# Performance work log

Hardware: AMD Instinct MI355X
Metric: run time of the kernel (lower is better)

Reference implementation:

```python
import jax, jax.numpy as jnp
import numpy as np
from jax import lax

NUM_VARS = 16384
NUM_CHECKS = 8192
BATCH = 32
MAX_ITER = 15
H_DENSITY = 0.001  # ~8 ones per column, LDPC-like Tanner graph


def setup_inputs() -> dict:
    key = jax.random.key(0)
    k_h, k_s, k_l = jax.random.split(key, 3)
    # Sparse binary parity-check matrix represented densely (same math).
    parity_matrix = (jax.random.uniform(k_h, (NUM_CHECKS, NUM_VARS)) < H_DENSITY).astype(jnp.float32)
    syndrome = jax.random.randint(k_s, (BATCH, NUM_CHECKS), 0, 2).astype(jnp.float32)
    channel_llrs = jax.random.normal(k_l, (BATCH, NUM_VARS), dtype=jnp.float32)
    w_vc = jnp.ones((1,), dtype=jnp.float32)
    w_cv = jnp.ones((1,), dtype=jnp.float32)
    damping = jnp.float32(0.5)
    return {
        "syndrome": syndrome,
        "parity_matrix": parity_matrix,
        "channel_llrs": channel_llrs,
        "w_vc": w_vc,
        "w_cv": w_cv,
        "damping": damping,
    }


def reference(syndrome, parity_matrix, channel_llrs, w_vc, w_cv, damping):
    # syndrome: (B, C); parity_matrix H: (C, V); channel_llrs: (B, V)
    s_sign = 1.0 - 2.0 * syndrome  # (B, C)

    def body(v_beliefs, _):
        # v -> c: sparse.mm(H, v^T)^T == v @ H^T  -> (B, C)
        v_to_c = w_vc * (v_beliefs @ parity_matrix.T)
        c_msg = s_sign * jnp.tanh(v_to_c * 0.5)  # (B, C)
        # c -> v: sparse.mm(H^T, c^T)^T == c @ H  -> (B, V)
        c_to_v = w_cv * (c_msg @ parity_matrix)
        v_new = damping * v_beliefs + (1.0 - damping) * (channel_llrs + c_to_v)
        return v_new, None

    v_beliefs, _ = lax.scan(body, channel_llrs, None, length=MAX_ITER)
    return jax.nn.sigmoid(-v_beliefs)  # (B, V) bit-flip probabilities
```

## Files before the change

### kernel.cpp

```cpp
#include <hip/hip_runtime.h>


#define C_NUM 8192
#define V_NUM 16384
#define B_NUM 32
#define ROW_SLOTS 40
#define COL_SLOTS 24

#define NBLK 256
#define NTHR 1024
#define NTH (NBLK * NTHR)

typedef unsigned short u16;
typedef unsigned int u32;
typedef unsigned long long u64;

#define ZERO_WORDS ((C_NUM * 4 + V_NUM * 4 + C_NUM * ROW_SLOTS * 2 + V_NUM * COL_SLOTS * 2) / 4)
#define NBAR 31

__device__ __forceinline__ float agent_ldf(const float* p) {
    return __hip_atomic_load(p, __ATOMIC_RELAXED, __HIP_MEMORY_SCOPE_AGENT);
}
__device__ __forceinline__ void agent_stf(float* p, float v) {
    __hip_atomic_store(p, v, __ATOMIC_RELAXED, __HIP_MEMORY_SCOPE_AGENT);
}
__device__ __forceinline__ void agent_st32(u32* p, u32 v) {
    __hip_atomic_store(p, v, __ATOMIC_RELAXED, __HIP_MEMORY_SCOPE_AGENT);
}
__device__ __forceinline__ void agent_st16(u16* p, u16 v) {
    __hip_atomic_store(p, v, __ATOMIC_RELAXED, __HIP_MEMORY_SCOPE_AGENT);
}

__device__ __forceinline__ void grid_barrier(u32* bars, int id) {
    __syncthreads();
    if (threadIdx.x == 0) {
        u32* base = bars + id * 512;
        asm volatile("s_waitcnt vmcnt(0) lgkmcnt(0)" ::: "memory");
        __hip_atomic_fetch_add(base + (blockIdx.x & 7) * 64, 1u,
                               __ATOMIC_RELAXED, __HIP_MEMORY_SCOPE_AGENT);
        u32 sum;
        do {
            sum = 0;
#pragma unroll
            for (int g = 0; g < 8; ++g)
                sum += __hip_atomic_load(base + g * 64,
                                         __ATOMIC_RELAXED, __HIP_MEMORY_SCOPE_AGENT);
            if (sum < (u32)NBLK) __builtin_amdgcn_s_sleep(2);
        } while (sum < (u32)NBLK);
        asm volatile("" ::: "memory");
    }
    __syncthreads();
}

__device__ __forceinline__ float fast_tanh_half(float x) {
    float ax = fabsf(x);
    float e = __expf(-ax);
    return copysignf((1.0f - e) / (1.0f + e), x);
}

__global__ __launch_bounds__(NTHR, 1)
void bp_fused(const float* __restrict__ H,
              const float* __restrict__ synd,
              const float* __restrict__ llr,
              const float* __restrict__ w_vc_p,
              const float* __restrict__ w_cv_p,
              const float* __restrict__ damp_p,
              int* __restrict__ row_cnt, int* __restrict__ col_cnt,
              u16* __restrict__ row_tab, u16* __restrict__ col_tab,
              float* __restrict__ bel, float* __restrict__ cms,
              u32* __restrict__ bars,
              float* __restrict__ out) {
    const int tid = blockIdx.x * NTHR + threadIdx.x;

    {
        u32* zp = (u32*)row_cnt;
        for (int t = tid; t < ZERO_WORDS; t += NTH) agent_st32(&zp[t], 0u);
        if (tid < 32) agent_stf(&bel[tid], 0.0f);
        else if (tid < 64) agent_stf(&cms[tid - 32], 0.0f);
    }
    float llr_r[2], bel_r[2];
#pragma unroll
    for (int r = 0; r < 2; ++r) {
        int i = tid + r * NTH;
        int b = i & 31, v = i >> 5;
        float x = llr[b * V_NUM + v];
        llr_r[r] = x; bel_r[r] = x;
        agent_stf(&bel[i + 32], x);
    }
    float ss_r;
    {
        int b = tid & 31, c = tid >> 5;
        ss_r = 1.0f - 2.0f * synd[b * C_NUM + c];
    }
    grid_barrier(bars, 0);

    {
        const int total4 = C_NUM * V_NUM / 4;
        const float4* Hv = (const float4*)H;
        for (int t = tid; t < total4; t += 2 * NTH) {
            float4 h0 = Hv[t];
            float4 h1 = Hv[t + NTH];
#pragma unroll
            for (int half = 0; half < 2; ++half) {
                float4 hv = half ? h1 : h0;
                int base = (half ? (t + NTH) : t) * 4;
                float vals[4] = {hv.x, hv.y, hv.z, hv.w};
#pragma unroll
                for (int k = 0; k < 4; ++k) {
                    if (vals[k] != 0.0f) {
                        int ee = base + k;
                        int c = ee >> 14;
                        int v = ee & (V_NUM - 1);
                        int rs = atomicAdd(&row_cnt[c], 1);
                        if (rs < ROW_SLOTS)
                            agent_st16(&row_tab[c * ROW_SLOTS + rs], (u16)(v + 1));
                        int cs = atomicAdd(&col_cnt[v], 1);
                        if (cs < COL_SLOTS)
                            agent_st16(&col_tab[v * COL_SLOTS + cs], (u16)(c + 1));
                    }
                }
            }
        }
    }
    grid_barrier(bars, 1);

    const float wvc = w_vc_p[0];
    const float wcv = w_cv_p[0];
    const float d   = damp_p[0];
    const int b  = tid & 31;
    const int c0 = tid >> 5;

    int barid = 2;
    for (int it = 0; it < 15; ++it) {
        {
            const u64* rt = (const u64*)(row_tab + (size_t)c0 * ROW_SLOTS);
            u64 w[10];
#pragma unroll
            for (int p = 0; p < 10; ++p) w[p] = rt[p];
            float sum = 0.0f;
#pragma unroll
            for (int p = 0; p < 10; ++p) {
                sum += agent_ldf(&bel[(int)(w[p] & 0xFFFFu) * 32 + b]);
                sum += agent_ldf(&bel[(int)((w[p] >> 16) & 0xFFFFu) * 32 + b]);
                sum += agent_ldf(&bel[(int)((w[p] >> 32) & 0xFFFFu) * 32 + b]);
                sum += agent_ldf(&bel[(int)(w[p] >> 48) * 32 + b]);
            }
            agent_stf(&cms[tid + 32], ss_r * fast_tanh_half(wvc * sum));
        }
        grid_barrier(bars, barid++);

        bool last = (it == 14);
#pragma unroll
        for (int r = 0; r < 2; ++r) {
            int i = tid + r * NTH;
            int v = i >> 5;
            const u64* ct = (const u64*)(col_tab + (size_t)v * COL_SLOTS);
            u64 w[6];
#pragma unroll
            for (int p = 0; p < 6; ++p) w[p] = ct[p];
            float sum = 0.0f;
#pragma unroll
            for (int p = 0; p < 6; ++p) {
                sum += agent_ldf(&cms[(int)(w[p] & 0xFFFFu) * 32 + b]);
                sum += agent_ldf(&cms[(int)((w[p] >> 16) & 0xFFFFu) * 32 + b]);
                sum += agent_ldf(&cms[(int)((w[p] >> 32) & 0xFFFFu) * 32 + b]);
                sum += agent_ldf(&cms[(int)(w[p] >> 48) * 32 + b]);
            }
            float nb = d * bel_r[r] + (1.0f - d) * (llr_r[r] + wcv * sum);
            bel_r[r] = nb;
            if (!last) agent_stf(&bel[i + 32], nb);
            else       out[b * V_NUM + v] = 1.0f / (1.0f + __expf(nb));
        }
        if (!last) grid_barrier(bars, barid++);
    }
}

extern "C" void kernel_launch(void* const* d_in, const int* in_sizes, int n_in,
                              void* d_out, int out_size, void* d_ws, size_t ws_size,
                              hipStream_t stream) {
    const float* synd = (const float*)d_in[0];
    const float* H    = (const float*)d_in[1];
    const float* llr  = (const float*)d_in[2];
    const float* w_vc = (const float*)d_in[3];
    const float* w_cv = (const float*)d_in[4];
    const float* damp = (const float*)d_in[5];
    float* out = (float*)d_out;

    char* ws = (char*)d_ws;
    size_t off = 0;
    int* row_cnt = (int*)(ws + off); off += (size_t)C_NUM * 4;
    int* col_cnt = (int*)(ws + off); off += (size_t)V_NUM * 4;
    u16* row_tab = (u16*)(ws + off); off += (size_t)C_NUM * ROW_SLOTS * 2;
    u16* col_tab = (u16*)(ws + off); off += (size_t)V_NUM * COL_SLOTS * 2;
    float* bel = (float*)(ws + off); off += (size_t)(V_NUM + 1) * 32 * 4;
    float* cms = (float*)(ws + off); off += (size_t)(C_NUM + 1) * 32 * 4;
    u32* bars  = (u32*)(ws + off); off += (size_t)NBAR * 512 * 4;

    hipMemsetAsync(bars, 0, (size_t)NBAR * 512 * 4, stream);

    void* args[] = {
        (void*)&H, (void*)&synd, (void*)&llr,
        (void*)&w_vc, (void*)&w_cv, (void*)&damp,
        (void*)&row_cnt, (void*)&col_cnt, (void*)&row_tab, (void*)&col_tab,
        (void*)&bel, (void*)&cms, (void*)&bars, (void*)&out
    };
    hipLaunchCooperativeKernel((const void*)bp_fused,
                               dim3(NBLK), dim3(NTHR), args, 0, stream);
}
```

Measured before the change: 1.071 ms.

## Replace counter grid barrier with per-block epoch flags and skip table zeroing

The atomic-counter grid barrier is replaced by one epoch flag per block, which 64 threads poll with a wave ballot. Only the row and column counts are zeroed now, not the whole adjacency tables. Unused table slots are filled with valid dummy indices, and their gathered values are masked out using per-row and per-column counts. This shortens barrier latency and start-up zeroing at the cost of one extra grid barrier and some select instructions. The launch_bounds change to 4 waves per SIMD also alters register allocation.

```diff
diff --git a/kernel.cpp b/kernel.cpp
--- a/kernel.cpp
+++ b/kernel.cpp
@@ -15,38 +15,42 @@
 typedef unsigned int u32;
 typedef unsigned long long u64;
 
-#define ZERO_WORDS ((C_NUM * 4 + V_NUM * 4 + C_NUM * ROW_SLOTS * 2 + V_NUM * COL_SLOTS * 2) / 4)
-#define NBAR 31
-
 __device__ __forceinline__ float agent_ldf(const float* p) {
     return __hip_atomic_load(p, __ATOMIC_RELAXED, __HIP_MEMORY_SCOPE_AGENT);
 }
 __device__ __forceinline__ void agent_stf(float* p, float v) {
     __hip_atomic_store(p, v, __ATOMIC_RELAXED, __HIP_MEMORY_SCOPE_AGENT);
 }
+__device__ __forceinline__ u32 agent_ld32(const u32* p) {
+    return __hip_atomic_load(p, __ATOMIC_RELAXED, __HIP_MEMORY_SCOPE_AGENT);
+}
 __device__ __forceinline__ void agent_st32(u32* p, u32 v) {
     __hip_atomic_store(p, v, __ATOMIC_RELAXED, __HIP_MEMORY_SCOPE_AGENT);
 }
+__device__ __forceinline__ int agent_ldi(const int* p) {
+    return __hip_atomic_load(p, __ATOMIC_RELAXED, __HIP_MEMORY_SCOPE_AGENT);
+}
 __device__ __forceinline__ void agent_st16(u16* p, u16 v) {
     __hip_atomic_store(p, v, __ATOMIC_RELAXED, __HIP_MEMORY_SCOPE_AGENT);
 }
 
-__device__ __forceinline__ void grid_barrier(u32* bars, int id) {
+__device__ __forceinline__ void grid_barrier(u32* flags, u32 ep) {
     __syncthreads();
-    if (threadIdx.x == 0) {
-        u32* base = bars + id * 512;
-        asm volatile("s_waitcnt vmcnt(0) lgkmcnt(0)" ::: "memory");
-        __hip_atomic_fetch_add(base + (blockIdx.x & 7) * 64, 1u,
-                               __ATOMIC_RELAXED, __HIP_MEMORY_SCOPE_AGENT);
-        u32 sum;
-        do {
-            sum = 0;
-#pragma unroll
-            for (int g = 0; g < 8; ++g)
-                sum += __hip_atomic_load(base + g * 64,
-                                         __ATOMIC_RELAXED, __HIP_MEMORY_SCOPE_AGENT);
-            if (sum < (u32)NBLK) __builtin_amdgcn_s_sleep(2);
-        } while (sum < (u32)NBLK);
+    if (threadIdx.x < 64) {
+        if (threadIdx.x == 0) {
+            asm volatile("s_waitcnt vmcnt(0) lgkmcnt(0)" ::: "memory");
+            agent_st32(&flags[blockIdx.x], ep);
+        }
+        const int base = threadIdx.x * 4;
+        for (;;) {
+            u32 f0 = agent_ld32(&flags[base + 0]);
+            u32 f1 = agent_ld32(&flags[base + 1]);
+            u32 f2 = agent_ld32(&flags[base + 2]);
+            u32 f3 = agent_ld32(&flags[base + 3]);
+            bool ok = (f0 >= ep) & (f1 >= ep) & (f2 >= ep) & (f3 >= ep);
+            if (__ballot(ok) == ~0ull) break;
+            __builtin_amdgcn_s_sleep(2);
+        }
         asm volatile("" ::: "memory");
     }
     __syncthreads();
@@ -58,7 +62,7 @@
     return copysignf((1.0f - e) / (1.0f + e), x);
 }
 
-__global__ __launch_bounds__(NTHR, 1)
+__global__ __launch_bounds__(NTHR, 4)
 void bp_fused(const float* __restrict__ H,
               const float* __restrict__ synd,
               const float* __restrict__ llr,
@@ -68,15 +72,14 @@
               int* __restrict__ row_cnt, int* __restrict__ col_cnt,
               u16* __restrict__ row_tab, u16* __restrict__ col_tab,
               float* __restrict__ bel, float* __restrict__ cms,
-              u32* __restrict__ bars,
+              u32* __restrict__ flags,
               float* __restrict__ out) {
     const int tid = blockIdx.x * NTHR + threadIdx.x;
+    u32 ep = 1;
 
     {
         u32* zp = (u32*)row_cnt;
-        for (int t = tid; t < ZERO_WORDS; t += NTH) agent_st32(&zp[t], 0u);
-        if (tid < 32) agent_stf(&bel[tid], 0.0f);
-        else if (tid < 64) agent_stf(&cms[tid - 32], 0.0f);
+        for (int t = tid; t < (C_NUM + V_NUM); t += NTH) agent_st32(&zp[t], 0u);
     }
     float llr_r[2], bel_r[2];
 #pragma unroll
@@ -92,7 +95,7 @@
         int b = tid & 31, c = tid >> 5;
         ss_r = 1.0f - 2.0f * synd[b * C_NUM + c];
     }
-    grid_barrier(bars, 0);
+    grid_barrier(flags, ep++);
 
     {
         const int total4 = C_NUM * V_NUM / 4;
@@ -122,32 +125,59 @@
             }
         }
     }
-    grid_barrier(bars, 1);
-
+    grid_barrier(flags, ep++);
+
+    if (tid < C_NUM) {
+        int c = tid;
+        int n = agent_ldi(&row_cnt[c]); n = n > ROW_SLOTS ? ROW_SLOTS : n;
+        for (int k = n; k < ROW_SLOTS; ++k)
+            agent_st16(&row_tab[c * ROW_SLOTS + k],
+                       (u16)((((c * 97) + (k * 131)) & (V_NUM - 1)) + 1));
+    } else if (tid < C_NUM + V_NUM) {
+        int v = tid - C_NUM;
+        int n = agent_ldi(&col_cnt[v]); n = n > COL_SLOTS ? COL_SLOTS : n;
+        for (int k = n; k < COL_SLOTS; ++k)
+            agent_st16(&col_tab[v * COL_SLOTS + k],
+                       (u16)((((v * 89) + (k * 61)) & (C_NUM - 1)) + 1));
+    }
     const float wvc = w_vc_p[0];
     const float wcv = w_cv_p[0];
     const float d   = damp_p[0];
     const int b  = tid & 31;
     const int c0 = tid >> 5;
-
-    int barid = 2;
+    int n_row;
+    {
+        int n = agent_ldi(&row_cnt[c0]);
+        n_row = n > ROW_SLOTS ? ROW_SLOTS : n;
+    }
+    int n_col[2];
+#pragma unroll
+    for (int r = 0; r < 2; ++r) {
+        int n = agent_ldi(&col_cnt[(tid + r * NTH) >> 5]);
+        n_col[r] = n > COL_SLOTS ? COL_SLOTS : n;
+    }
+    grid_barrier(flags, ep++);
+
     for (int it = 0; it < 15; ++it) {
         {
             const u64* rt = (const u64*)(row_tab + (size_t)c0 * ROW_SLOTS);
-            u64 w[10];
-#pragma unroll
-            for (int p = 0; p < 10; ++p) w[p] = rt[p];
             float sum = 0.0f;
 #pragma unroll
-            for (int p = 0; p < 10; ++p) {
-                sum += agent_ldf(&bel[(int)(w[p] & 0xFFFFu) * 32 + b]);
-                sum += agent_ldf(&bel[(int)((w[p] >> 16) & 0xFFFFu) * 32 + b]);
-                sum += agent_ldf(&bel[(int)((w[p] >> 32) & 0xFFFFu) * 32 + b]);
-                sum += agent_ldf(&bel[(int)(w[p] >> 48) * 32 + b]);
+            for (int p = 0; p < ROW_SLOTS / 4; ++p) {
+                u64 q = rt[p];
+                float v0 = agent_ldf(&bel[(int)(q & 0xFFFFu) * 32 + b]);
+                float v1 = agent_ldf(&bel[(int)((q >> 16) & 0xFFFFu) * 32 + b]);
+                float v2 = agent_ldf(&bel[(int)((q >> 32) & 0xFFFFu) * 32 + b]);
+                float v3 = agent_ldf(&bel[(int)(q >> 48) * 32 + b]);
+                int j = p * 4;
+                sum += (j     < n_row) ? v0 : 0.0f;
+                sum += (j + 1 < n_row) ? v1 : 0.0f;
+                sum += (j + 2 < n_row) ? v2 : 0.0f;
+                sum += (j + 3 < n_row) ? v3 : 0.0f;
             }
             agent_stf(&cms[tid + 32], ss_r * fast_tanh_half(wvc * sum));
         }
-        grid_barrier(bars, barid++);
+        grid_barrier(flags, ep++);
 
         bool last = (it == 14);
 #pragma unroll
@@ -155,23 +185,26 @@
             int i = tid + r * NTH;
             int v = i >> 5;
             const u64* ct = (const u64*)(col_tab + (size_t)v * COL_SLOTS);
-            u64 w[6];
-#pragma unroll
-            for (int p = 0; p < 6; ++p) w[p] = ct[p];
             float sum = 0.0f;
 #pragma unroll
-            for (int p = 0; p < 6; ++p) {
-                sum += agent_ldf(&cms[(int)(w[p] & 0xFFFFu) * 32 + b]);
-                sum += agent_ldf(&cms[(int)((w[p] >> 16) & 0xFFFFu) * 32 + b]);
-                sum += agent_ldf(&cms[(int)((w[p] >> 32) & 0xFFFFu) * 32 + b]);
-                sum += agent_ldf(&cms[(int)(w[p] >> 48) * 32 + b]);
+            for (int p = 0; p < COL_SLOTS / 4; ++p) {
+                u64 q = ct[p];
+                float v0 = agent_ldf(&cms[(int)(q & 0xFFFFu) * 32 + b]);
+                float v1 = agent_ldf(&cms[(int)((q >> 16) & 0xFFFFu) * 32 + b]);
+                float v2 = agent_ldf(&cms[(int)((q >> 32) & 0xFFFFu) * 32 + b]);
+                float v3 = agent_ldf(&cms[(int)(q >> 48) * 32 + b]);
+                int j = p * 4;
+                sum += (j     < n_col[r]) ? v0 : 0.0f;
+                sum += (j + 1 < n_col[r]) ? v1 : 0.0f;
+                sum += (j + 2 < n_col[r]) ? v2 : 0.0f;
+                sum += (j + 3 < n_col[r]) ? v3 : 0.0f;
             }
             float nb = d * bel_r[r] + (1.0f - d) * (llr_r[r] + wcv * sum);
             bel_r[r] = nb;
             if (!last) agent_stf(&bel[i + 32], nb);
             else       out[b * V_NUM + v] = 1.0f / (1.0f + __expf(nb));
         }
-        if (!last) grid_barrier(bars, barid++);
+        if (!last) grid_barrier(flags, ep++);
     }
 }
 
@@ -194,15 +227,15 @@
     u16* col_tab = (u16*)(ws + off); off += (size_t)V_NUM * COL_SLOTS * 2;
     float* bel = (float*)(ws + off); off += (size_t)(V_NUM + 1) * 32 * 4;
     float* cms = (float*)(ws + off); off += (size_t)(C_NUM + 1) * 32 * 4;
-    u32* bars  = (u32*)(ws + off); off += (size_t)NBAR * 512 * 4;
-
-    hipMemsetAsync(bars, 0, (size_t)NBAR * 512 * 4, stream);
+    u32* flags = (u32*)(ws + off); off += (size_t)NBLK * 4;
+
+    hipMemsetAsync(flags, 0, (size_t)NBLK * 4, stream);
 
     void* args[] = {
         (void*)&H, (void*)&synd, (void*)&llr,
         (void*)&w_vc, (void*)&w_cv, (void*)&damp,
         (void*)&row_cnt, (void*)&col_cnt, (void*)&row_tab, (void*)&col_tab,
-        (void*)&bel, (void*)&cms, (void*)&bars, (void*)&out
+        (void*)&bel, (void*)&cms, (void*)&flags, (void*)&out
     };
     hipLaunchCooperativeKernel((const void*)bp_fused,
                                dim3(NBLK), dim3(NTHR), args, 0, stream);
```

Result: faster. 1.031 ms (-3.7%).
